# Optimization experiments

Measured on AMD Instinct MI355X. Metric: run time of the kernel, lower is better.

Reference implementation:

```python
import jax, jax.numpy as jnp
from jax import lax
import numpy as np

B, S, D = 32, 2048, 512

def setup_inputs() -> dict:
    key = jax.random.key(0)
    ks = jax.random.split(key, 9)
    inv = 1.0 / np.sqrt(D).astype(np.float32)
    return {
        "query": jax.random.normal(ks[0], (B, 1, D), jnp.float32),
        "value": jax.random.normal(ks[1], (B, S, D), jnp.float32),
        "last_alignment_energy": jax.random.uniform(ks[2], (B, S), jnp.float32),
        "conv_w": jax.random.normal(ks[3], (D, 1, 3), jnp.float32) * 0.1,  # Conv1d(1->D,k=3)
        "conv_b": jax.random.normal(ks[4], (D,), jnp.float32) * 0.01,
        "w_q": jax.random.normal(ks[5], (D, D), jnp.float32) * inv,  # applied as x @ w_q
        "w_v": jax.random.normal(ks[6], (D, D), jnp.float32) * inv,
        "bias": jax.random.uniform(ks[7], (D,), jnp.float32, minval=-0.1, maxval=0.1),
        "score_w": jax.random.normal(ks[8], (D,), jnp.float32) * inv,  # score_proj weight (out=1)
        "score_b": jnp.zeros((), jnp.float32),
    }


def reference(query, value, last_alignment_energy, conv_w, conv_b, w_q, w_v, bias, score_w, score_b):
    # location features: Conv1d(1->D, k=3, pad=1) over the previous alignment
    loc = lax.conv_general_dilated(
        last_alignment_energy[:, None, :], conv_w,
        window_strides=(1,), padding=[(1, 1)],
        dimension_numbers=("NCH", "OIH", "NCH"))  # [B, D, S]
    loc = jnp.transpose(loc, (0, 2, 1)) + conv_b  # [B, S, D]

    # additive attention energy: tanh(Wq q + Wv v + loc + b) @ score_w
    hidden = jnp.tanh(query @ w_q + value @ w_v + loc + bias)  # [B, S, D] (query broadcasts over S)
    scores = hidden @ score_w + score_b                          # [B, S]
    align = jax.nn.softmax(scores, axis=-1)                      # [B, S]

    # context = align^T V
    context = jnp.einsum("bs,bsd->bd", align, value)             # [B, D]
    return context, align
```

## Files before the change

kernel.cpp:

```cpp
#include <hip/hip_runtime.h>
#include <hip/hip_bf16.h>

#define B_ 32
#define S_ 2048
#define D_ 512
#define M_ (B_*S_)

typedef __bf16 bf16x8 __attribute__((ext_vector_type(8)));
typedef float  f32x4  __attribute__((ext_vector_type(4)));

__device__ __forceinline__ float tanh_fast(float x){
  float e2 = __expf(2.f * x);
  return 1.f - 2.f * __builtin_amdgcn_rcpf(e2 + 1.f);
}

__device__ __forceinline__ bf16x8 cvt8(f32x4 a, f32x4 b){
  bf16x8 t;
  t[0]=(__bf16)a[0]; t[1]=(__bf16)a[1]; t[2]=(__bf16)a[2]; t[3]=(__bf16)a[3];
  t[4]=(__bf16)b[0]; t[5]=(__bf16)b[1]; t[6]=(__bf16)b[2]; t[7]=(__bf16)b[3];
  return t;
}

__global__ void k_reorder_wv(const float* __restrict__ wv,
                             unsigned short* __restrict__ wvr){
  int frag = blockIdx.x;
  int lane = threadIdx.x;
  int ks = frag >> 5, nt = frag & 31;
  int k0 = ks*32 + (lane>>4)*8;
  int d  = nt*16 + (lane&15);
  bf16x8 t;
  #pragma unroll
  for (int j=0;j<8;++j) t[j] = (__bf16)wv[(k0+j)*D_ + d];
  *reinterpret_cast<uint4*>(wvr + ((size_t)frag*64 + lane)*8) =
      __builtin_bit_cast(uint4, t);
}

__global__ void k_qproj(const float* __restrict__ q,
                        const float* __restrict__ wq,
                        const float* __restrict__ bias,
                        float* __restrict__ qp){
  int b  = blockIdx.y;
  int t  = threadIdx.x;
  int dl = t & 127, eg = t >> 7;
  int d  = blockIdx.x*128 + dl;
  __shared__ float qs[D_];
  __shared__ float red[4][128];
  for (int e=t; e<D_; e+=512) qs[e] = q[b*D_+e];
  __syncthreads();
  float acc = 0.f;
  #pragma unroll 8
  for (int i=0;i<128;++i){
    int e = eg*128 + i;
    acc = fmaf(qs[e], wq[(size_t)e*D_+d], acc);
  }
  red[eg][dl] = acc;
  __syncthreads();
  if (eg == 0)
    qp[b*D_+d] = red[0][dl]+red[1][dl]+red[2][dl]+red[3][dl] + bias[d];
}

__launch_bounds__(256, 2)
__global__ void k_energy(const float* __restrict__ value,
                         const unsigned short* __restrict__ wvr,
                         const float* __restrict__ qp,
                         const float* __restrict__ energy,
                         const float* __restrict__ conv_w,
                         const float* __restrict__ conv_b,
                         const float* __restrict__ score_w,
                         float* __restrict__ scores){
  const int t    = threadIdx.x;
  const int wave = t >> 6;
  const int lane = t & 63;
  const int quad = lane >> 4;
  const int lm   = lane & 15;
  const int row0 = blockIdx.x * 64;
  const int b    = row0 >> 11;
  const int s0   = row0 & (S_-1);

  f32x4 acc[4][8];
  #pragma unroll
  for (int mt=0;mt<4;++mt)
    #pragma unroll
    for (int nt=0;nt<8;++nt)
      acc[mt][nt] = (f32x4){0.f,0.f,0.f,0.f};

  const float* aP = value + (size_t)(row0+lm)*D_ + quad*8;
  const unsigned short* bP = wvr + ((size_t)(wave*8)*64 + lane)*8;

  f32x4 aN[4][2];
  #pragma unroll
  for (int mt=0;mt<4;++mt){
    const float* p = aP + (size_t)mt*16*D_;
    aN[mt][0] = *reinterpret_cast<const f32x4*>(p);
    aN[mt][1] = *reinterpret_cast<const f32x4*>(p+4);
  }

  for (int kc=0; kc<15; ++kc){
    bf16x8 af[4];
    #pragma unroll
    for (int mt=0;mt<4;++mt) af[mt] = cvt8(aN[mt][0], aN[mt][1]);
    #pragma unroll
    for (int mt=0;mt<4;++mt){
      const float* p = aP + (size_t)mt*16*D_ + (kc+1)*32;
      aN[mt][0] = *reinterpret_cast<const f32x4*>(p);
      aN[mt][1] = *reinterpret_cast<const f32x4*>(p+4);
    }
    #pragma unroll
    for (int ntl=0;ntl<8;++ntl){
      bf16x8 bf = __builtin_bit_cast(bf16x8,
        *reinterpret_cast<const uint4*>(bP + (size_t)(kc*32+ntl)*512));
      #pragma unroll
      for (int mt=0;mt<4;++mt)
        acc[mt][ntl] = __builtin_amdgcn_mfma_f32_16x16x32_bf16(af[mt], bf, acc[mt][ntl], 0,0,0);
    }
  }
  {
    bf16x8 af[4];
    #pragma unroll
    for (int mt=0;mt<4;++mt) af[mt] = cvt8(aN[mt][0], aN[mt][1]);
    #pragma unroll
    for (int ntl=0;ntl<8;++ntl){
      bf16x8 bf = __builtin_bit_cast(bf16x8,
        *reinterpret_cast<const uint4*>(bP + (size_t)(15*32+ntl)*512));
      #pragma unroll
      for (int mt=0;mt<4;++mt)
        acc[mt][ntl] = __builtin_amdgcn_mfma_f32_16x16x32_bf16(af[mt], bf, acc[mt][ntl], 0,0,0);
    }
  }

  float sw[8], c0[8], c1[8], c2[8], cb[8], qv[8];
  #pragma unroll
  for (int ntl=0; ntl<8; ++ntl){
    int d = wave*128 + ntl*16 + lm;
    sw[ntl] = score_w[d];
    c0[ntl] = conv_w[d*3+0];
    c1[ntl] = conv_w[d*3+1];
    c2[ntl] = conv_w[d*3+2];
    cb[ntl] = conv_b[d];
    qv[ntl] = qp[b*D_+d];
  }
  __shared__ float red[4][64];
  const float* eB = energy + b*S_;
  #pragma unroll
  for (int mt=0; mt<4; ++mt){
    #pragma unroll
    for (int r=0;r<4;++r){
      int sl = mt*16 + quad*4 + r;
      int s  = s0 + sl;
      float em1 = (s > 0)    ? eB[s-1] : 0.f;
      float e0  =              eB[s];
      float ep1 = (s < S_-1) ? eB[s+1] : 0.f;
      float p = 0.f;
      #pragma unroll
      for (int ntl=0; ntl<8; ++ntl){
        float h = acc[mt][ntl][r] + qv[ntl]
                + fmaf(c0[ntl],em1, fmaf(c1[ntl],e0, fmaf(c2[ntl],ep1, cb[ntl])));
        p = fmaf(sw[ntl], tanh_fast(h), p);
      }
      #pragma unroll
      for (int m=1; m<16; m<<=1) p += __shfl_xor(p, m, 64);
      if (lm == 0) red[wave][sl] = p;
    }
  }
  __syncthreads();
  if (t < 64)
    scores[row0 + t] = red[0][t] + red[1][t] + red[2][t] + red[3][t];
}

__launch_bounds__(512)
__global__ void k_ctx(const float* __restrict__ scores,
                      const float* __restrict__ value,
                      float* __restrict__ out_align,
                      float* __restrict__ cpart){
  int b = blockIdx.y, sc = blockIdx.x;
  int t = threadIdx.x;
  int lane = t & 63, wid = t >> 6;
  __shared__ float redm[8], reds[8];
  __shared__ float als[128];

  float v[4], mx = -3.4e38f;
  #pragma unroll
  for (int i=0;i<4;++i){
    v[i] = scores[b*S_ + t + i*512];
    mx = fmaxf(mx, v[i]);
  }
  #pragma unroll
  for (int m=1;m<64;m<<=1) mx = fmaxf(mx, __shfl_xor(mx, m, 64));
  if (lane==0) redm[wid] = mx;
  __syncthreads();
  #pragma unroll
  for (int w=0;w<8;++w) mx = fmaxf(mx, redm[w]);
  float sum = 0.f;
  #pragma unroll
  for (int i=0;i<4;++i) sum += __expf(v[i]-mx);
  #pragma unroll
  for (int m=1;m<64;m<<=1) sum += __shfl_xor(sum, m, 64);
  if (lane==0) reds[wid] = sum;
  __syncthreads();
  sum = 0.f;
  #pragma unroll
  for (int w=0;w<8;++w) sum += reds[w];
  float inv = 1.f/sum;

  if (t < 128){
    float a = __expf(scores[b*S_ + sc*128 + t] - mx) * inv;
    out_align[b*S_ + sc*128 + t] = a;
    als[t] = a;
  }
  __syncthreads();

  int r = t >> 7;
  int c = (t & 127) * 4;
  f32x4 acc = (f32x4){0.f,0.f,0.f,0.f};
  #pragma unroll 8
  for (int i=0;i<32;++i){
    int sl = i*4 + r;
    float al = als[sl];
    f32x4 vv = *reinterpret_cast<const f32x4*>(
                 value + ((size_t)(b*S_ + sc*128 + sl))*D_ + c);
    acc += al * vv;
  }
  __shared__ float lred[4][D_];
  #pragma unroll
  for (int j=0;j<4;++j) lred[r][c+j] = acc[j];
  __syncthreads();
  if (r == 0){
    #pragma unroll
    for (int j=0;j<4;++j)
      cpart[((size_t)(b*16+sc))*D_ + c + j] =
          lred[0][c+j] + lred[1][c+j] + lred[2][c+j] + lred[3][c+j];
  }
}

__global__ void k_ctx_reduce(const float* __restrict__ cpart,
                             float* __restrict__ out_ctx){
  int idx = blockIdx.x*256 + threadIdx.x;
  int b = idx >> 9, d = idx & 511;
  float s = 0.f;
  #pragma unroll
  for (int j=0;j<16;++j) s += cpart[((size_t)(b*16+j))*D_ + d];
  out_ctx[idx] = s;
}

extern "C" void kernel_launch(void* const* d_in, const int* in_sizes, int n_in,
                              void* d_out, int out_size, void* d_ws, size_t ws_size,
                              hipStream_t stream){
  const float* query   = (const float*)d_in[0];
  const float* value   = (const float*)d_in[1];
  const float* energy  = (const float*)d_in[2];
  const float* conv_w  = (const float*)d_in[3];
  const float* conv_b  = (const float*)d_in[4];
  const float* w_q     = (const float*)d_in[5];
  const float* w_v     = (const float*)d_in[6];
  const float* bias    = (const float*)d_in[7];
  const float* score_w = (const float*)d_in[8];

  char* ws = (char*)d_ws;
  unsigned short* wvr = (unsigned short*)(ws);
  float* qp     = (float*)(ws + (512<<10));
  float* scores = (float*)(ws + (576<<10));
  float* cpart  = (float*)(ws + (832<<10));

  float* out_ctx   = (float*)d_out;
  float* out_align = out_ctx + B_*D_;

  k_reorder_wv<<<dim3(512),      dim3(64),  0, stream>>>(w_v, wvr);
  k_qproj     <<<dim3(4,32),     dim3(512), 0, stream>>>(query, w_q, bias, qp);
  k_energy    <<<dim3(M_/64),    dim3(256), 0, stream>>>(value, wvr, qp, energy,
                                                         conv_w, conv_b, score_w, scores);
  k_ctx       <<<dim3(16,B_),    dim3(512), 0, stream>>>(scores, value, out_align, cpart);
  k_ctx_reduce<<<dim3(B_*D_/256),dim3(256), 0, stream>>>(cpart, out_ctx);
}
```

Before: 310.2 us.

## Prefetch B fragments with phase-staggered K order, merge prelude kernels, atomic context reduce

The energy GEMM now double-buffers the weight fragments in registers, and each block starts its K loop at a different phase so concurrent blocks read different weight slices. The W_v reorder and query projection are merged into one launch. The context kernel uses smaller 256-thread blocks with 64 rows each and accumulates into the output with atomics after a memset, which removes the separate reduction kernel. These changes target launch overhead and memory-latency stalls, at the cost of more register pressure and a nondeterministic atomic summation order.

```diff
diff --git a/kernel.cpp b/kernel.cpp
--- a/kernel.cpp
+++ b/kernel.cpp
@@ -8,6 +8,7 @@
 
 typedef __bf16 bf16x8 __attribute__((ext_vector_type(8)));
 typedef float  f32x4  __attribute__((ext_vector_type(4)));
+typedef unsigned int u32x4 __attribute__((ext_vector_type(4)));
 
 __device__ __forceinline__ float tanh_fast(float x){
   float e2 = __expf(2.f * x);
@@ -21,42 +22,49 @@
   return t;
 }
 
-__global__ void k_reorder_wv(const float* __restrict__ wv,
-                             unsigned short* __restrict__ wvr){
-  int frag = blockIdx.x;
-  int lane = threadIdx.x;
-  int ks = frag >> 5, nt = frag & 31;
-  int k0 = ks*32 + (lane>>4)*8;
-  int d  = nt*16 + (lane&15);
-  bf16x8 t;
-  #pragma unroll
-  for (int j=0;j<8;++j) t[j] = (__bf16)wv[(k0+j)*D_ + d];
-  *reinterpret_cast<uint4*>(wvr + ((size_t)frag*64 + lane)*8) =
-      __builtin_bit_cast(uint4, t);
-}
-
-__global__ void k_qproj(const float* __restrict__ q,
-                        const float* __restrict__ wq,
-                        const float* __restrict__ bias,
-                        float* __restrict__ qp){
-  int b  = blockIdx.y;
-  int t  = threadIdx.x;
-  int dl = t & 127, eg = t >> 7;
-  int d  = blockIdx.x*128 + dl;
+__device__ __forceinline__ bf16x8 ldB(const unsigned short* p){
+  u32x4 u = __builtin_nontemporal_load((const u32x4*)p);
+  return __builtin_bit_cast(bf16x8, u);
+}
+
+__global__ void k_prelude(const float* __restrict__ wv,
+                          unsigned short* __restrict__ wvr,
+                          const float* __restrict__ q,
+                          const float* __restrict__ wq,
+                          const float* __restrict__ bias,
+                          float* __restrict__ qp){
   __shared__ float qs[D_];
-  __shared__ float red[4][128];
-  for (int e=t; e<D_; e+=512) qs[e] = q[b*D_+e];
-  __syncthreads();
-  float acc = 0.f;
-  #pragma unroll 8
-  for (int i=0;i<128;++i){
-    int e = eg*128 + i;
-    acc = fmaf(qs[e], wq[(size_t)e*D_+d], acc);
-  }
-  red[eg][dl] = acc;
-  __syncthreads();
-  if (eg == 0)
-    qp[b*D_+d] = red[0][dl]+red[1][dl]+red[2][dl]+red[3][dl] + bias[d];
+  __shared__ float red[2][128];
+  int t = threadIdx.x;
+  if (blockIdx.x < 128){
+    int frag = blockIdx.x*4 + (t>>6);
+    int lane = t & 63;
+    int ks = frag >> 5, nt = frag & 31;
+    int k0 = ks*32 + ((lane>>4)&3)*8;
+    int d  = nt*16 + (lane&15);
+    bf16x8 v;
+    #pragma unroll
+    for (int j=0;j<8;++j) v[j] = (__bf16)wv[(k0+j)*D_ + d];
+    *reinterpret_cast<uint4*>(wvr + ((size_t)frag*64 + lane)*8) =
+        __builtin_bit_cast(uint4, v);
+  } else {
+    int j  = blockIdx.x - 128;
+    int b  = j >> 2, dg = j & 3;
+    int dl = t & 127, eg = t >> 7;
+    int d  = dg*128 + dl;
+    for (int e=t; e<D_; e+=256) qs[e] = q[b*D_+e];
+    __syncthreads();
+    float acc = 0.f;
+    #pragma unroll 8
+    for (int i=0;i<256;++i){
+      int e = eg*256 + i;
+      acc = fmaf(qs[e], wq[(size_t)e*D_+d], acc);
+    }
+    red[eg][dl] = acc;
+    __syncthreads();
+    if (eg == 0)
+      qp[b*D_+d] = red[0][dl] + red[1][dl] + bias[d];
+  }
 }
 
 __launch_bounds__(256, 2)
@@ -76,6 +84,7 @@
   const int row0 = blockIdx.x * 64;
   const int b    = row0 >> 11;
   const int s0   = row0 & (S_-1);
+  const int phase = blockIdx.x & 15;
 
   f32x4 acc[4][8];
   #pragma unroll
@@ -87,57 +96,59 @@
   const float* aP = value + (size_t)(row0+lm)*D_ + quad*8;
   const unsigned short* bP = wvr + ((size_t)(wave*8)*64 + lane)*8;
 
-  f32x4 aN[4][2];
-  #pragma unroll
-  for (int mt=0;mt<4;++mt){
-    const float* p = aP + (size_t)mt*16*D_;
-    aN[mt][0] = *reinterpret_cast<const f32x4*>(p);
-    aN[mt][1] = *reinterpret_cast<const f32x4*>(p+4);
-  }
-
-  for (int kc=0; kc<15; ++kc){
-    bf16x8 af[4];
-    #pragma unroll
-    for (int mt=0;mt<4;++mt) af[mt] = cvt8(aN[mt][0], aN[mt][1]);
+  f32x4  aN[4][2];
+  bf16x8 bC[8], bN[8];
+  {
+    const int k0 = phase;
     #pragma unroll
     for (int mt=0;mt<4;++mt){
-      const float* p = aP + (size_t)mt*16*D_ + (kc+1)*32;
+      const float* p = aP + (size_t)mt*16*D_ + k0*32;
       aN[mt][0] = *reinterpret_cast<const f32x4*>(p);
       aN[mt][1] = *reinterpret_cast<const f32x4*>(p+4);
     }
     #pragma unroll
-    for (int ntl=0;ntl<8;++ntl){
-      bf16x8 bf = __builtin_bit_cast(bf16x8,
-        *reinterpret_cast<const uint4*>(bP + (size_t)(kc*32+ntl)*512));
-      #pragma unroll
-      for (int mt=0;mt<4;++mt)
-        acc[mt][ntl] = __builtin_amdgcn_mfma_f32_16x16x32_bf16(af[mt], bf, acc[mt][ntl], 0,0,0);
-    }
-  }
-  {
+    for (int nt=0;nt<8;++nt)
+      bC[nt] = ldB(bP + (size_t)(k0*32+nt)*512);
+  }
+
+  #pragma unroll
+  for (int u=0; u<16; ++u){
+    const int kn = (u + 1 + phase) & 15;
     bf16x8 af[4];
     #pragma unroll
     for (int mt=0;mt<4;++mt) af[mt] = cvt8(aN[mt][0], aN[mt][1]);
-    #pragma unroll
-    for (int ntl=0;ntl<8;++ntl){
-      bf16x8 bf = __builtin_bit_cast(bf16x8,
-        *reinterpret_cast<const uint4*>(bP + (size_t)(15*32+ntl)*512));
-      #pragma unroll
-      for (int mt=0;mt<4;++mt)
-        acc[mt][ntl] = __builtin_amdgcn_mfma_f32_16x16x32_bf16(af[mt], bf, acc[mt][ntl], 0,0,0);
+    if (u < 15){
+      #pragma unroll
+      for (int mt=0;mt<4;++mt){
+        const float* p = aP + (size_t)mt*16*D_ + kn*32;
+        aN[mt][0] = *reinterpret_cast<const f32x4*>(p);
+        aN[mt][1] = *reinterpret_cast<const f32x4*>(p+4);
+      }
+      #pragma unroll
+      for (int nt=0;nt<8;++nt)
+        bN[nt] = ldB(bP + (size_t)(kn*32+nt)*512);
+    }
+    #pragma unroll
+    for (int mt=0;mt<4;++mt)
+      #pragma unroll
+      for (int nt=0;nt<8;++nt)
+        acc[mt][nt] = __builtin_amdgcn_mfma_f32_16x16x32_bf16(af[mt], bC[nt], acc[mt][nt], 0,0,0);
+    if (u < 15){
+      #pragma unroll
+      for (int nt=0;nt<8;++nt) bC[nt] = bN[nt];
     }
   }
 
   float sw[8], c0[8], c1[8], c2[8], cb[8], qv[8];
   #pragma unroll
-  for (int ntl=0; ntl<8; ++ntl){
-    int d = wave*128 + ntl*16 + lm;
-    sw[ntl] = score_w[d];
-    c0[ntl] = conv_w[d*3+0];
-    c1[ntl] = conv_w[d*3+1];
-    c2[ntl] = conv_w[d*3+2];
-    cb[ntl] = conv_b[d];
-    qv[ntl] = qp[b*D_+d];
+  for (int nt=0; nt<8; ++nt){
+    int d = wave*128 + nt*16 + lm;
+    sw[nt] = score_w[d];
+    c0[nt] = conv_w[d*3+0];
+    c1[nt] = conv_w[d*3+1];
+    c2[nt] = conv_w[d*3+2];
+    cb[nt] = conv_b[d];
+    qv[nt] = qp[b*D_+d];
   }
   __shared__ float red[4][64];
   const float* eB = energy + b*S_;
@@ -152,10 +163,10 @@
       float ep1 = (s < S_-1) ? eB[s+1] : 0.f;
       float p = 0.f;
       #pragma unroll
-      for (int ntl=0; ntl<8; ++ntl){
-        float h = acc[mt][ntl][r] + qv[ntl]
-                + fmaf(c0[ntl],em1, fmaf(c1[ntl],e0, fmaf(c2[ntl],ep1, cb[ntl])));
-        p = fmaf(sw[ntl], tanh_fast(h), p);
+      for (int nt=0; nt<8; ++nt){
+        float h = acc[mt][nt][r] + qv[nt]
+                + fmaf(c0[nt],em1, fmaf(c1[nt],e0, fmaf(c2[nt],ep1, cb[nt])));
+        p = fmaf(sw[nt], tanh_fast(h), p);
       }
       #pragma unroll
       for (int m=1; m<16; m<<=1) p += __shfl_xor(p, m, 64);
@@ -167,79 +178,67 @@
     scores[row0 + t] = red[0][t] + red[1][t] + red[2][t] + red[3][t];
 }
 
-__launch_bounds__(512)
+__launch_bounds__(256)
 __global__ void k_ctx(const float* __restrict__ scores,
                       const float* __restrict__ value,
                       float* __restrict__ out_align,
-                      float* __restrict__ cpart){
+                      float* __restrict__ out_ctx){
   int b = blockIdx.y, sc = blockIdx.x;
   int t = threadIdx.x;
   int lane = t & 63, wid = t >> 6;
-  __shared__ float redm[8], reds[8];
-  __shared__ float als[128];
-
-  float v[4], mx = -3.4e38f;
-  #pragma unroll
-  for (int i=0;i<4;++i){
-    v[i] = scores[b*S_ + t + i*512];
+  __shared__ float redm[4], reds[4];
+  __shared__ float als[64];
+  __shared__ float lred[4][D_];
+
+  float v[8], mx = -3.4e38f;
+  #pragma unroll
+  for (int i=0;i<8;++i){
+    v[i] = scores[b*S_ + t + i*256];
     mx = fmaxf(mx, v[i]);
   }
   #pragma unroll
   for (int m=1;m<64;m<<=1) mx = fmaxf(mx, __shfl_xor(mx, m, 64));
   if (lane==0) redm[wid] = mx;
   __syncthreads();
-  #pragma unroll
-  for (int w=0;w<8;++w) mx = fmaxf(mx, redm[w]);
+  mx = fmaxf(fmaxf(redm[0],redm[1]), fmaxf(redm[2],redm[3]));
   float sum = 0.f;
   #pragma unroll
-  for (int i=0;i<4;++i) sum += __expf(v[i]-mx);
+  for (int i=0;i<8;++i) sum += __expf(v[i]-mx);
   #pragma unroll
   for (int m=1;m<64;m<<=1) sum += __shfl_xor(sum, m, 64);
   if (lane==0) reds[wid] = sum;
   __syncthreads();
-  sum = 0.f;
-  #pragma unroll
-  for (int w=0;w<8;++w) sum += reds[w];
+  sum = reds[0]+reds[1]+reds[2]+reds[3];
   float inv = 1.f/sum;
 
-  if (t < 128){
-    float a = __expf(scores[b*S_ + sc*128 + t] - mx) * inv;
-    out_align[b*S_ + sc*128 + t] = a;
+  if (t < 64){
+    float a = __expf(scores[b*S_ + sc*64 + t] - mx) * inv;
+    out_align[b*S_ + sc*64 + t] = a;
     als[t] = a;
   }
   __syncthreads();
 
-  int r = t >> 7;
-  int c = (t & 127) * 4;
-  f32x4 acc = (f32x4){0.f,0.f,0.f,0.f};
-  #pragma unroll 8
-  for (int i=0;i<32;++i){
+  int r = t >> 6;
+  int c = (t & 63) * 8;
+  f32x4 a0 = (f32x4){0.f,0.f,0.f,0.f};
+  f32x4 a1 = (f32x4){0.f,0.f,0.f,0.f};
+  #pragma unroll 4
+  for (int i=0;i<16;++i){
     int sl = i*4 + r;
     float al = als[sl];
-    f32x4 vv = *reinterpret_cast<const f32x4*>(
-                 value + ((size_t)(b*S_ + sc*128 + sl))*D_ + c);
-    acc += al * vv;
-  }
-  __shared__ float lred[4][D_];
-  #pragma unroll
-  for (int j=0;j<4;++j) lred[r][c+j] = acc[j];
+    const float* vp = value + ((size_t)(b*S_ + sc*64 + sl))*D_ + c;
+    a0 += al * *reinterpret_cast<const f32x4*>(vp);
+    a1 += al * *reinterpret_cast<const f32x4*>(vp+4);
+  }
+  #pragma unroll
+  for (int j=0;j<4;++j){ lred[r][c+j] = a0[j]; lred[r][c+4+j] = a1[j]; }
   __syncthreads();
   if (r == 0){
     #pragma unroll
-    for (int j=0;j<4;++j)
-      cpart[((size_t)(b*16+sc))*D_ + c + j] =
-          lred[0][c+j] + lred[1][c+j] + lred[2][c+j] + lred[3][c+j];
-  }
-}
-
-__global__ void k_ctx_reduce(const float* __restrict__ cpart,
-                             float* __restrict__ out_ctx){
-  int idx = blockIdx.x*256 + threadIdx.x;
-  int b = idx >> 9, d = idx & 511;
-  float s = 0.f;
-  #pragma unroll
-  for (int j=0;j<16;++j) s += cpart[((size_t)(b*16+j))*D_ + d];
-  out_ctx[idx] = s;
+    for (int j=0;j<8;++j)
+      atomicAdd(&out_ctx[b*D_ + c + j],
+                lred[0][c+j] + lred[1][c+j] + lred[2][c+j] + lred[3][c+j]);
+  }
 }
 
 extern "C" void kernel_launch(void* const* d_in, const int* in_sizes, int n_in,
@@ -259,15 +258,13 @@
   unsigned short* wvr = (unsigned short*)(ws);
   float* qp     = (float*)(ws + (512<<10));
   float* scores = (float*)(ws + (576<<10));
-  float* cpart  = (float*)(ws + (832<<10));
 
   float* out_ctx   = (float*)d_out;
   float* out_align = out_ctx + B_*D_;
 
-  k_reorder_wv<<<dim3(512),      dim3(64),  0, stream>>>(w_v, wvr);
-  k_qproj     <<<dim3(4,32),     dim3(512), 0, stream>>>(query, w_q, bias, qp);
-  k_energy    <<<dim3(M_/64),    dim3(256), 0, stream>>>(value, wvr, qp, energy,
-                                                         conv_w, conv_b, score_w, scores);
-  k_ctx       <<<dim3(16,B_),    dim3(512), 0, stream>>>(scores, value, out_align, cpart);
-  k_ctx_reduce<<<dim3(B_*D_/256),dim3(256), 0, stream>>>(cpart, out_ctx);
-}
+  hipMemsetAsync(out_ctx, 0, (size_t)B_*D_*sizeof(float), stream);
+  k_prelude<<<dim3(256),     dim3(256), 0, stream>>>(w_v, wvr, query, w_q, bias, qp);
+  k_energy <<<dim3(M_/64),   dim3(256), 0, stream>>>(value, wvr, qp, energy,
+                                                     conv_w, conv_b, score_w, scores);
+  k_ctx    <<<dim3(32,B_),   dim3(256), 0, stream>>>(scores, value, out_align, out_ctx);
+}
```

Result: slower. 333.4 us (+7.5%).
